# Kernel tuning notes

Measured on AMD Instinct MI355X. Metric: run time of the kernel, lower is better.

## Reference

```python
import jax, jax.numpy as jnp
import numpy as np

B, T, C = 2, 2048, 1024
H, GAMMA = 16, 8
D = C // H
SCALE = 1.0 / np.sqrt(D).astype(np.float32)


def setup_inputs() -> dict:
    key = jax.random.key(0)
    ks = jax.random.split(key, 6)
    w = 0.02
    return {
        'x': jax.random.normal(ks[0], (B, T, C), dtype=jnp.float32),
        'Wq': jax.random.normal(ks[1], (C, 2 * C), dtype=jnp.float32) * w,
        'Wk': jax.random.normal(ks[2], (C, 2 * C), dtype=jnp.float32) * w,
        'Wv': jax.random.normal(ks[3], (C, C), dtype=jnp.float32) * w,
        'Wo': jax.random.normal(ks[4], (C, C), dtype=jnp.float32) * w,
        'theta_offset': jax.random.normal(ks[5], (H,), dtype=jnp.float32) * 0.1,
    }


def _heads(t):
    # (B, T, C) -> (B, H, T, D)
    return t.reshape(B, T, H, D).transpose(0, 2, 1, 3)


def reference(x, Wq, Wk, Wv, Wo, theta_offset):
    q_raw = x @ Wq                      # (B, T, 2C)
    k_raw = x @ Wk                      # (B, T, 2C)
    v = _heads(x @ Wv)                  # (B, H, T, D)

    q_amp, q_phase = jnp.split(q_raw, 2, axis=-1)
    k_amp, k_phase = jnp.split(k_raw, 2, axis=-1)
    q_amp = jax.nn.softplus(_heads(q_amp))
    q_phase = _heads(q_phase)
    k_amp = jax.nn.softplus(_heads(k_amp))
    k_phase = _heads(k_phase)

    q_real = q_amp * jnp.cos(q_phase)
    q_imag = q_amp * jnp.sin(q_phase)
    k_real = k_amp * jnp.cos(k_phase)
    k_imag = k_amp * jnp.sin(k_phase)

    scores = (jnp.einsum('bhtd,bhsd->bhts', q_real, k_real)
              + jnp.einsum('bhtd,bhsd->bhts', q_imag, k_imag)) * SCALE

    # theta gating (active since T > GAMMA)
    cycle_ids = jnp.arange(T, dtype=jnp.float32) / GAMMA
    cycle_dist = cycle_ids[None, :] - cycle_ids[:, None]        # (T, T)
    theta_gate = jnp.cos(theta_offset[:, None, None] * cycle_dist)  # (H, T, T)
    scores = scores * theta_gate[None]

    causal = jnp.tril(jnp.ones((T, T), dtype=bool))
    scores = jnp.where(causal[None, None], scores, -jnp.inf)
    attn = jax.nn.softmax(scores, axis=-1)

    out = jnp.einsum('bhts,bhsd->bhtd', attn, v)
    out = out.transpose(0, 2, 1, 3).reshape(B, T, C)
    return out @ Wo
```

## Files before the change

kernel.cpp:

```cpp
#include <hip/hip_runtime.h>
#include <hip/hip_bf16.h>
#include <math.h>

#define Bc 2
#define Tc 2048
#define Cc 1024
#define Hc 16
#define Dc 64

typedef __attribute__((ext_vector_type(8))) short short8;
typedef __attribute__((ext_vector_type(4))) float f32x4;

#define L2E 1.44269504088896f
#define SM_M 20.0f

__device__ __forceinline__ short f2bf(float x) {
    unsigned u = __float_as_uint(x);
    u += 0x7fff + ((u >> 16) & 1);
    return (short)(u >> 16);
}
__device__ __forceinline__ unsigned pack2bf_fast(float a, float b) {
    unsigned ua = __float_as_uint(a) + 0x8000u;
    unsigned ub = __float_as_uint(b) + 0x8000u;
    return __builtin_amdgcn_perm(ub, ua, 0x07060302);
}
__device__ __forceinline__ float softplus_fast(float a) {
    return fmaxf(a, 0.f) + __logf(1.f + __expf(-fabsf(a)));
}

#define RDA(BUF, MH) do {                                                      \
    const short* Ah_ = &Al[BUF][MH][0];                                        \
    _Pragma("unroll") for (int mt_ = 0; mt_ < 4; ++mt_) {                      \
        af[mt_][0] = *(const short8*)&Ah_[(wm*64 + mt_*16 + c)*64 + rsw0];     \
        af[mt_][1] = *(const short8*)&Ah_[(wm*64 + mt_*16 + c)*64 + rsw1];     \
    } } while (0)

#define RDB(BUF, NH) do {                                                      \
    const short* Bh_ = &Bl[BUF][NH][0];                                        \
    _Pragma("unroll") for (int nf_ = 0; nf_ < 2; ++nf_) {                      \
        bfr[NH][nf_][0] = *(const short8*)&Bh_[(wn*32 + nf_*16 + c)*64 + rsw0];\
        bfr[NH][nf_][1] = *(const short8*)&Bh_[(wn*32 + nf_*16 + c)*64 + rsw1];\
    } } while (0)

#define MMQ(MH, NH) do {                                                       \
    _Pragma("unroll") for (int mt_ = 0; mt_ < 4; ++mt_)                        \
    _Pragma("unroll") for (int nf_ = 0; nf_ < 2; ++nf_) {                      \
        acc[MH][NH][mt_][nf_] = __builtin_amdgcn_mfma_f32_16x16x32_bf16(       \
            af[mt_][0], bfr[NH][nf_][0], acc[MH][NH][mt_][nf_], 0, 0, 0);      \
        acc[MH][NH][mt_][nf_] = __builtin_amdgcn_mfma_f32_16x16x32_bf16(       \
            af[mt_][1], bfr[NH][nf_][1], acc[MH][NH][mt_][nf_], 0, 0, 0);      \
    } } while (0)

#define BARw asm volatile("s_barrier" ::: "memory")
#define VMW6 asm volatile("s_waitcnt vmcnt(6)" ::: "memory")
#define VMW0 asm volatile("s_waitcnt vmcnt(0)" ::: "memory")
#define PRIO1 __builtin_amdgcn_s_setprio(1)
#define PRIO0 __builtin_amdgcn_s_setprio(0)

__global__ __launch_bounds__(512, 2) void gemm256_qk(
    const short* __restrict__ A, const short* __restrict__ Bt,
    short* __restrict__ q2, short* __restrict__ k2)
{
    __shared__ __attribute__((aligned(16))) short Al[2][2][128 * 64];
    __shared__ __attribute__((aligned(16))) short Bl[2][2][128 * 64];

    const int tid = threadIdx.x;
    const int wave = tid >> 6, lane = tid & 63;
    const int quad = lane >> 4, c = lane & 15;
    const int wm = wave >> 2, wn = wave & 3;
    const int m0 = blockIdx.y * 256, n0 = blockIdx.x * 256;

    const int rsw0 = ((quad * 16) ^ ((c & 7) << 4)) >> 1;
    const int rsw1 = ((64 + quad * 16) ^ ((c & 7) << 4)) >> 1;

    f32x4 acc[2][2][4][2];
#pragma unroll
    for (int a0 = 0; a0 < 2; ++a0)
#pragma unroll
        for (int a1 = 0; a1 < 2; ++a1)
#pragma unroll
            for (int a2 = 0; a2 < 4; ++a2)
#pragma unroll
                for (int a3 = 0; a3 < 2; ++a3)
                    acc[a0][a1][a2][a3] = (f32x4){0.f, 0.f, 0.f, 0.f};

    short8 af[4][2];
    short8 bfr[2][2][2];

    auto stA = [&](int kt, int hh) {
        short* dstb = &Al[kt & 1][hh][0];
#pragma unroll
        for (int j = 0; j < 2; ++j) {
            int ch = j * 512 + tid;
            int row = ch >> 3;
            int os = ((((ch & 7) << 4) ^ ((row & 7) << 4)) >> 1);
            const short* src = A + (size_t)(m0 + hh * 128 + row) * 1024 + kt * 64 + os;
            __builtin_amdgcn_global_load_lds(
                (const __attribute__((address_space(1))) void*)src,
                (__attribute__((address_space(3))) void*)(dstb + (j * 512 + wave * 64) * 8),
                16, 0, 0);
        }
    };
    auto stB = [&](int kt, int hh) {
        short* dstb = &Bl[kt & 1][hh][0];
#pragma unroll
        for (int j = 0; j < 2; ++j) {
            int ch = j * 512 + tid;
            int row = ch >> 3;
            int os = ((((ch & 7) << 4) ^ ((row & 7) << 4)) >> 1);
            const short* src = Bt + (size_t)(n0 + hh * 128 + row) * 1024 + kt * 64 + os;
            __builtin_amdgcn_global_load_lds(
                (const __attribute__((address_space(1))) void*)src,
                (__attribute__((address_space(3))) void*)(dstb + (j * 512 + wave * 64) * 8),
                16, 0, 0);
        }
    };

    stB(0, 0); stA(0, 0); stB(0, 1); stA(0, 1); stB(1, 0); stA(1, 0); stB(1, 1);
    VMW6;
    BARw;

    for (int i = 0; i < 8; ++i) {
        const int e = 2 * i;
        const bool more = (i < 7);
        RDA(0, 0); RDB(0, 0);
        stA(e + 1, 1);
        BARw; PRIO1; MMQ(0, 0); PRIO0; BARw;
        RDB(0, 1);
        if (more) stB(e + 2, 0);
        BARw; PRIO1; MMQ(0, 1); PRIO0; BARw;
        RDA(0, 1);
        if (more) stA(e + 2, 0);
        BARw; PRIO1; MMQ(1, 0); PRIO0; BARw;
        if (more) stB(e + 2, 1);
        BARw; PRIO1; MMQ(1, 1); PRIO0;
        if (more) { VMW6; } else { VMW0; }
        BARw;
        RDA(1, 0); RDB(1, 0);
        if (more) stA(e + 2, 1);
        BARw; PRIO1; MMQ(0, 0); PRIO0; BARw;
        RDB(1, 1);
        if (more) stB(e + 3, 0);
        BARw; PRIO1; MMQ(0, 1); PRIO0; BARw;
        RDA(1, 1);
        if (more) stA(e + 3, 0);
        BARw; PRIO1; MMQ(1, 0); PRIO0; BARw;
        if (more) stB(e + 3, 1);
        BARw; PRIO1; MMQ(1, 1); PRIO0;
        if (more) { VMW6; } else { VMW0; }
        BARw;
    }

    const int bx = blockIdx.x;
    const int d = wn * 16 + c;
#pragma unroll
    for (int mh = 0; mh < 2; ++mh) {
#pragma unroll
        for (int nh = 0; nh < 2; ++nh) {
            const int g = 2 * bx + nh;
            const int isK = g >> 4;
            const int hh = g & 15;
            const float scl = isK ? 1.f : 0.125f;
            short* dst = isK ? k2 : q2;
#pragma unroll
            for (int mt = 0; mt < 4; ++mt) {
#pragma unroll
                for (int reg = 0; reg < 4; ++reg) {
                    int m = m0 + mh * 128 + wm * 64 + mt * 16 + quad * 4 + reg;
                    int bb = m >> 11, tt = m & (Tc - 1);
                    size_t base = (((size_t)bb * Hc + hh) * Tc + tt) * 128;
                    float amp = acc[mh][nh][mt][0][reg];
                    float ph  = acc[mh][nh][mt][1][reg];
                    float sp = softplus_fast(amp) * scl;
                    float sn, cs;
                    __sincosf(ph, &sn, &cs);
                    dst[base + d]      = f2bf(sp * cs);
                    dst[base + d + 64] = f2bf(sp * sn);
                }
            }
        }
    }
}

template <int EPI>
__global__ __launch_bounds__(256) void gemm_bt_mfma(
    const short* __restrict__ A, const short* __restrict__ Bt,
    float* __restrict__ Cf, short* __restrict__ Cb,
    int M, int N, int K)
{
    __shared__ __attribute__((aligned(16))) short As[128 * 32];
    __shared__ __attribute__((aligned(16))) short Bs[128 * 32];

    const int tid = threadIdx.x;
    const int wave = tid >> 6, lane = tid & 63;
    const int quad = lane >> 4, c = lane & 15;
    const int wm = wave >> 1, wn = wave & 1;
    const int m0 = blockIdx.y * 128, n0 = blockIdx.x * 128;

    const int srow = lane >> 2;
    const int scol = (lane & 3) * 8;
    const short* Ag = A  + (size_t)(m0 + wave * 32 + srow) * K + scol;
    const short* Bg = Bt + (size_t)(n0 + wave * 32 + srow) * K + scol;
    short* AsW = As + (wave * 32) * 32;
    short* BsW = Bs + (wave * 32) * 32;

    f32x4 acc[4][4];
#pragma unroll
    for (int i = 0; i < 4; ++i)
#pragma unroll
        for (int j = 0; j < 4; ++j)
            acc[i][j] = (f32x4){0.f, 0.f, 0.f, 0.f};

    for (int k0 = 0; k0 < K; k0 += 32) {
        __syncthreads();
#pragma unroll
        for (int i = 0; i < 2; ++i) {
            __builtin_amdgcn_global_load_lds(
                (const __attribute__((address_space(1))) void*)(Ag + k0 + (size_t)i * 16 * K),
                (__attribute__((address_space(3))) void*)(AsW + i * 16 * 32), 16, 0, 0);
            __builtin_amdgcn_global_load_lds(
                (const __attribute__((address_space(1))) void*)(Bg + k0 + (size_t)i * 16 * K),
                (__attribute__((address_space(3))) void*)(BsW + i * 16 * 32), 16, 0, 0);
        }
        __syncthreads();

        short8 af[4], bf[4];
#pragma unroll
        for (int mt = 0; mt < 4; ++mt)
            af[mt] = *(const short8*)&As[(wm * 64 + mt * 16 + c) * 32 + quad * 8];
#pragma unroll
        for (int nt = 0; nt < 4; ++nt)
            bf[nt] = *(const short8*)&Bs[(wn * 64 + nt * 16 + c) * 32 + quad * 8];
#pragma unroll
        for (int mt = 0; mt < 4; ++mt)
#pragma unroll
            for (int nt = 0; nt < 4; ++nt)
                acc[mt][nt] = __builtin_amdgcn_mfma_f32_16x16x32_bf16(
                    af[mt], bf[nt], acc[mt][nt], 0, 0, 0);
    }

#pragma unroll
    for (int mt = 0; mt < 4; ++mt) {
#pragma unroll
        for (int reg = 0; reg < 4; ++reg) {
            size_t row = m0 + wm * 64 + mt * 16 + quad * 4 + reg;
#pragma unroll
            for (int nt = 0; nt < 4; ++nt) {
                size_t col = n0 + wn * 64 + nt * 16 + c;
                if (EPI == 1) Cb[row * N + col] = f2bf(acc[mt][nt][reg]);
                else          Cf[row * N + col] = acc[mt][nt][reg];
            }
        }
    }
}

__global__ __launch_bounds__(256) void gemm_v2t(
    const short* __restrict__ A, const short* __restrict__ Bt,
    short* __restrict__ v2t)
{
    __shared__ __attribute__((aligned(16))) short As[128 * 32];
    __shared__ __attribute__((aligned(16))) short Bs[128 * 32];
    __shared__ __attribute__((aligned(16))) short tile[128 * 136];

    const int K = Cc;
    const int tid = threadIdx.x;
    const int wave = tid >> 6, lane = tid & 63;
    const int quad = lane >> 4, c = lane & 15;
    const int wm = wave >> 1, wn = wave & 1;
    const int m0 = blockIdx.y * 128, n0 = blockIdx.x * 128;

    const int srow = lane >> 2;
    const int scol = (lane & 3) * 8;
    const short* Ag = A  + (size_t)(m0 + wave * 32 + srow) * K + scol;
    const short* Bg = Bt + (size_t)(n0 + wave * 32 + srow) * K + scol;
    short* AsW = As + (wave * 32) * 32;
    short* BsW = Bs + (wave * 32) * 32;

    f32x4 acc[4][4];
#pragma unroll
    for (int i = 0; i < 4; ++i)
#pragma unroll
        for (int j = 0; j < 4; ++j)
            acc[i][j] = (f32x4){0.f, 0.f, 0.f, 0.f};

    for (int k0 = 0; k0 < K; k0 += 32) {
        __syncthreads();
#pragma unroll
        for (int i = 0; i < 2; ++i) {
            __builtin_amdgcn_global_load_lds(
                (const __attribute__((address_space(1))) void*)(Ag + k0 + (size_t)i * 16 * K),
                (__attribute__((address_space(3))) void*)(AsW + i * 16 * 32), 16, 0, 0);
            __builtin_amdgcn_global_load_lds(
                (const __attribute__((address_space(1))) void*)(Bg + k0 + (size_t)i * 16 * K),
                (__attribute__((address_space(3))) void*)(BsW + i * 16 * 32), 16, 0, 0);
        }
        __syncthreads();

        short8 af[4], bf[4];
#pragma unroll
        for (int mt = 0; mt < 4; ++mt)
            af[mt] = *(const short8*)&As[(wm * 64 + mt * 16 + c) * 32 + quad * 8];
#pragma unroll
        for (int nt = 0; nt < 4; ++nt)
            bf[nt] = *(const short8*)&Bs[(wn * 64 + nt * 16 + c) * 32 + quad * 8];
#pragma unroll
        for (int mt = 0; mt < 4; ++mt)
#pragma unroll
            for (int nt = 0; nt < 4; ++nt)
                acc[mt][nt] = __builtin_amdgcn_mfma_f32_16x16x32_bf16(
                    af[mt], bf[nt], acc[mt][nt], 0, 0, 0);
    }

#pragma unroll
    for (int mt = 0; mt < 4; ++mt)
#pragma unroll
        for (int reg = 0; reg < 4; ++reg) {
            int tl = wm * 64 + mt * 16 + quad * 4 + reg;
#pragma unroll
            for (int nt = 0; nt < 4; ++nt)
                tile[(wn * 64 + nt * 16 + c) * 136 + tl] = f2bf(acc[mt][nt][reg]);
        }
    __syncthreads();

    const int b = m0 >> 11, tl0 = m0 & (Tc - 1);
#pragma unroll
    for (int i = 0; i < 8; ++i) {
        int n = i * 16 + (tid >> 4);
        int t8 = (tid & 15) * 8;
        int ng = n0 + n, h = ng >> 6, d = ng & 63;
        *(short8*)&v2t[(((size_t)b * Hc + h) * Dc + d) * Tc + tl0 + t8] =
            *(const short8*)&tile[n * 136 + t8];
    }
}

__global__ __launch_bounds__(256) void xconv(const float* __restrict__ x,
                                             short* __restrict__ xb)
{
    int idx = blockIdx.x * 256 + threadIdx.x;
    float4 v = *(const float4*)&x[(size_t)idx * 4];
    short4 o = {f2bf(v.x), f2bf(v.y), f2bf(v.z), f2bf(v.w)};
    *(short4*)&xb[(size_t)idx * 4] = o;
}

__global__ __launch_bounds__(256) void wtrans_qk(const float* __restrict__ Wq,
                                                 const float* __restrict__ Wk,
                                                 short* __restrict__ Bt)
{
    __shared__ short tile[64][80];
    const int n0 = blockIdx.x * 64, k0 = blockIdx.y * 64;
    const int half = blockIdx.z;
    const float* W = half ? Wk : Wq;
    const int tid = threadIdx.x;
#pragma unroll
    for (int i = 0; i < 4; ++i) {
        int e = i * 256 + tid;
        int k = e >> 4, n4 = (e & 15) * 4;
        float4 v = *(const float4*)&W[(size_t)(k0 + k) * 2048 + n0 + n4];
        tile[k][n4]     = f2bf(v.x);
        tile[k][n4 + 1] = f2bf(v.y);
        tile[k][n4 + 2] = f2bf(v.z);
        tile[k][n4 + 3] = f2bf(v.w);
    }
    __syncthreads();
#pragma unroll
    for (int i = 0; i < 16; ++i) {
        int e = i * 256 + tid;
        int n = e >> 6, k = e & 63;
        int ng = n0 + n;
        int sub = ng >> 10, hh = (ng >> 6) & 15, dd = ng & 63;
        int r = (half * 16 + hh) * 128 + (dd >> 4) * 32 + sub * 16 + (dd & 15);
        Bt[(size_t)r * Cc + k0 + k] = tile[k][n];
    }
}

__global__ __launch_bounds__(256) void wtrans2(const float* __restrict__ Wv,
                                               const float* __restrict__ Wo,
                                               short* __restrict__ WtBase)
{
    __shared__ short tile[64][80];
    const int n0 = blockIdx.x * 64, k0 = blockIdx.y * 64;
    const float* W = blockIdx.z ? Wo : Wv;
    short* Wt = WtBase + (size_t)blockIdx.z * Cc * Cc;
    const int tid = threadIdx.x;
#pragma unroll
    for (int i = 0; i < 4; ++i) {
        int e = i * 256 + tid;
        int k = e >> 4, n4 = (e & 15) * 4;
        float4 v = *(const float4*)&W[(size_t)(k0 + k) * Cc + n0 + n4];
        tile[k][n4]     = f2bf(v.x);
        tile[k][n4 + 1] = f2bf(v.y);
        tile[k][n4 + 2] = f2bf(v.z);
        tile[k][n4 + 3] = f2bf(v.w);
    }
    __syncthreads();
#pragma unroll
    for (int i = 0; i < 16; ++i) {
        int e = i * 256 + tid;
        int n = e >> 6, k = e & 63;
        Wt[(size_t)(n0 + n) * Cc + k0 + k] = tile[k][n];
    }
}

__global__ __launch_bounds__(512, 4) void moire_attn6(
    const short* __restrict__ q2, const short* __restrict__ k2,
    const short* __restrict__ v2t, const float* __restrict__ theta,
    short* __restrict__ att)
{
    __shared__ __attribute__((aligned(16))) short Ks[2][64 * 128];
    __shared__ __attribute__((aligned(16))) short Vt[2][64 * 64];
    __shared__ __attribute__((aligned(16))) short Ps[8][16 * 64];

    const int tid = threadIdx.x;
    const int wave = tid >> 6, lane = tid & 63;
    const int quad = lane >> 4, c = lane & 15;
    const int tx = wave >> 2, wq = wave & 3;
    const int p = blockIdx.x, h = blockIdx.y, b = blockIdx.z;
    const int qx = tx ? (31 - p) : p;
    const int q0 = qx * 64;
    const float th = theta[h];

    const short* k2b = k2 + (size_t)(b * Hc + h) * Tc * 128;
    const short* v2b = v2t + (size_t)(b * Hc + h) * Dc * Tc;

    short8 qf[4];
    const short* qp = q2 + ((size_t)(b * Hc + h) * Tc + q0 + wq * 16 + c) * 128;
#pragma unroll
    for (int i = 0; i < 4; ++i)
        qf[i] = *(const short8*)(qp + i * 32 + quad * 8);

    const int t_l = wq * 16 + c;
    float x0 = th * 0.125f * (float)(q0 + t_l);
    float cb = __cosf(x0), sb = -__sinf(x0);
    float cOff[4][4], sOff[4][4];
#pragma unroll
    for (int mt = 0; mt < 4; ++mt)
#pragma unroll
        for (int reg = 0; reg < 4; ++reg) {
            float a = th * 0.125f * (float)(mt * 16 + quad * 4 + reg);
            cOff[mt][reg] = __cosf(a) * L2E;
            sOff[mt][reg] = __sinf(a) * L2E;
        }
    const float cD = __cosf(8.f * th), sD = __sinf(8.f * th);

    f32x4 oacc[4];
    float lsum = 0.f;
#pragma unroll
    for (int nt = 0; nt < 4; ++nt)
        oacc[nt] = (f32x4){0.f, 0.f, 0.f, 0.f};

    auto stageK = [&](int jts) {
        short* KsB = &Ks[jts & 1][0];
        const int s0 = jts * 64;
#pragma unroll
        for (int i = 0; i < 2; ++i) {
            int ch = i * 512 + tid;
            int row = ch >> 4, j = ch & 15;
            const short* src = k2b + (size_t)(s0 + row) * 128 + ((j ^ (row & 15)) << 3);
            __builtin_amdgcn_global_load_lds(
                (const __attribute__((address_space(1))) void*)src,
                (__attribute__((address_space(3))) void*)(KsB + (i * 512 + wave * 64) * 8),
                16, 0, 0);
        }
    };
    auto stageV = [&](int jts) {
        short* VtB = &Vt[jts & 1][0];
        const int s0 = jts * 64;
        int row = tid >> 3, j = tid & 7;
        const short* src = v2b + (size_t)row * Tc + s0 + ((j ^ (row & 7)) << 3);
        __builtin_amdgcn_global_load_lds(
            (const __attribute__((address_space(1))) void*)src,
            (__attribute__((address_space(3))) void*)(VtB + (wave * 64) * 8),
            16, 0, 0);
    };

    auto do_pv = [&](int jprev) {
        const short* VtB = &Vt[jprev & 1][0];
        short8 pf[2];
#pragma unroll
        for (int kk = 0; kk < 2; ++kk)
            pf[kk] = *(const short8*)&Ps[wave][c * 64 +
                         (((kk * 4 + quad) ^ (c & 7)) << 3)];
#pragma unroll
        for (int nt = 0; nt < 4; ++nt)
#pragma unroll
            for (int kk = 0; kk < 2; ++kk) {
                short8 vf = *(const short8*)&VtB[(nt * 16 + c) * 64 +
                             (((kk * 4 + quad) ^ (c & 7)) << 3)];
                oacc[nt] = __builtin_amdgcn_mfma_f32_16x16x32_bf16(
                    pf[kk], vf, oacc[nt], 0, 0, 0);
            }
    };

    auto do_s = [&](int jt) {
        const short* KsB = &Ks[jt & 1][0];
        const bool diag = (jt == qx);

        f32x4 s_acc[4];
#pragma unroll
        for (int mt = 0; mt < 4; ++mt) {
            f32x4 a = {0.f, 0.f, 0.f, 0.f};
#pragma unroll
            for (int kk = 0; kk < 4; ++kk) {
                short8 kf = *(const short8*)&KsB[(mt * 16 + c) * 128 +
                                                 (((kk * 4 + quad) ^ c) << 3)];
                a = __builtin_amdgcn_mfma_f32_16x16x32_bf16(kf, qf[kk], a, 0, 0, 0);
            }
            s_acc[mt] = a;
        }

#pragma unroll
        for (int mt = 0; mt < 4; ++mt) {
            float pv[4];
#pragma unroll
            for (int reg = 0; reg < 4; ++reg) {
                float g2 = cb * cOff[mt][reg] - sb * sOff[mt][reg];
                float arg = fmaf(s_acc[mt][reg], g2, -SM_M * L2E);
                if (diag && (mt * 16 + quad * 4 + reg) > t_l) arg = -1e30f;
                pv[reg] = exp2f(arg);
            }
            lsum += (pv[0] + pv[1]) + (pv[2] + pv[3]);
            uint2 pk = {pack2bf_fast(pv[0], pv[1]), pack2bf_fast(pv[2], pv[3])};
            int slot = ((mt * 2 + (quad >> 1)) ^ (c & 7));
            *(uint2*)&Ps[wave][c * 64 + slot * 8 + (quad & 1) * 4] = pk;
        }

        float ncb = cb * cD - sb * sD;
        sb = sb * cD + cb * sD;
        cb = ncb;
    };

    stageK(0);
    const int jtEnd = 31 - p;
    for (int jt = 0; jt <= jtEnd; ++jt) {
        __syncthreads();
        if (jt < jtEnd) stageK(jt + 1);
        stageV(jt);

        const bool doS  = (jt <= qx);
        const bool doPV = (jt >= 1) & (jt <= qx + 1);
        if (doS & doPV) {
            do_pv(jt - 1);
            do_s(jt);
        } else if (doS) {
            do_s(jt);
        } else if (doPV) {
            do_pv(jt - 1);
        }
    }

    __syncthreads();
    if (qx == jtEnd) do_pv(jtEnd);

    float l = lsum;
    l += __shfl_xor(l, 16);
    l += __shfl_xor(l, 32);
    float il = 1.f / l;
    float ilr[4];
#pragma unroll
    for (int reg = 0; reg < 4; ++reg)
        ilr[reg] = __shfl(il, quad * 4 + reg);
#pragma unroll
    for (int reg = 0; reg < 4; ++reg) {
        int t_g = q0 + wq * 16 + quad * 4 + reg;
#pragma unroll
        for (int nt = 0; nt < 4; ++nt)
            att[(size_t)(b * Tc + t_g) * Cc + h * Dc + nt * 16 + c] =
                f2bf(oacc[nt][reg] * ilr[reg]);
    }
}

extern "C" void kernel_launch(void* const* d_in, const int* in_sizes, int n_in,
                              void* d_out, int out_size, void* d_ws, size_t ws_size,
                              hipStream_t stream)
{
    const float* x     = (const float*)d_in[0];
    const float* Wq    = (const float*)d_in[1];
    const float* Wk    = (const float*)d_in[2];
    const float* Wv    = (const float*)d_in[3];
    const float* Wo    = (const float*)d_in[4];
    const float* theta = (const float*)d_in[5];
    float* out = (float*)d_out;

    const int M = Bc * Tc;
    char* ws = (char*)d_ws;
    const size_t MB = 1 << 20;
    short* xb   = (short*)(ws);
    short* Bqk  = (short*)(ws + 8 * MB);
    short* Wvt  = (short*)(ws + 16 * MB);
    short* Wot  = (short*)(ws + 18 * MB);
    short* v2t  = (short*)(ws + 28 * MB);
    short* attb = (short*)(ws + 36 * MB);
    short* q2   = (short*)(ws + 44 * MB);
    short* k2   = (short*)d_out;

    xconv<<<(size_t)M * Cc / 1024, 256, 0, stream>>>(x, xb);
    wtrans_qk<<<dim3(2048 / 64, Cc / 64, 2), 256, 0, stream>>>(Wq, Wk, Bqk);
    wtrans2<<<dim3(Cc / 64, Cc / 64, 2), 256, 0, stream>>>(Wv, Wo, Wvt);

    gemm256_qk<<<dim3(4096 / 256, M / 256), 512, 0, stream>>>(xb, Bqk, q2, k2);
    gemm_v2t<<<dim3(Cc / 128, M / 128), 256, 0, stream>>>(xb, Wvt, v2t);

    moire_attn6<<<dim3(16, Hc, Bc), 512, 0, stream>>>(q2, k2, v2t, theta, attb);

    gemm_bt_mfma<0><<<dim3(Cc / 128, M / 128), 256, 0, stream>>>(
        attb, Wot, out, nullptr, M, Cc, Cc);
}
```

Baseline: 245.9 us.

## Split attention KV range across two wave groups per query tile

```diff
diff --git a/kernel.cpp b/kernel.cpp
--- a/kernel.cpp
+++ b/kernel.cpp
@@ -401,21 +401,21 @@
     }
 }
 
-__global__ __launch_bounds__(512, 4) void moire_attn6(
+__global__ __launch_bounds__(512, 4) void moire_attn7(
     const short* __restrict__ q2, const short* __restrict__ k2,
     const short* __restrict__ v2t, const float* __restrict__ theta,
     short* __restrict__ att)
 {
-    __shared__ __attribute__((aligned(16))) short Ks[2][64 * 128];
-    __shared__ __attribute__((aligned(16))) short Vt[2][64 * 64];
-    __shared__ __attribute__((aligned(16))) short Ps[8][16 * 64];
+    __shared__ __attribute__((aligned(16))) short Ks[2][2][32 * 128];
+    __shared__ __attribute__((aligned(16))) short Vt[2][2][64 * 32];
+    __shared__ __attribute__((aligned(16))) short Ps[8][16 * 32];
 
     const int tid = threadIdx.x;
     const int wave = tid >> 6, lane = tid & 63;
     const int quad = lane >> 4, c = lane & 15;
-    const int tx = wave >> 2, wq = wave & 3;
-    const int p = blockIdx.x, h = blockIdx.y, b = blockIdx.z;
-    const int qx = tx ? (31 - p) : p;
+    const int tx = wave >> 2, gw = wave & 3;
+    const int qx = 31 - blockIdx.x;
+    const int h = blockIdx.y, b = blockIdx.z;
     const int q0 = qx * 64;
     const float th = theta[h];
 
@@ -423,24 +423,26 @@
     const short* v2b = v2t + (size_t)(b * Hc + h) * Dc * Tc;
 
     short8 qf[4];
-    const short* qp = q2 + ((size_t)(b * Hc + h) * Tc + q0 + wq * 16 + c) * 128;
+    const short* qp = q2 + ((size_t)(b * Hc + h) * Tc + q0 + gw * 16 + c) * 128;
 #pragma unroll
     for (int i = 0; i < 4; ++i)
         qf[i] = *(const short8*)(qp + i * 32 + quad * 8);
 
-    const int t_l = wq * 16 + c;
-    float x0 = th * 0.125f * (float)(q0 + t_l);
-    float cb = __cosf(x0), sb = -__sinf(x0);
-    float cOff[4][4], sOff[4][4];
-#pragma unroll
-    for (int mt = 0; mt < 4; ++mt)
+    const int t_l = gw * 16 + c;
+    const int t_g = q0 + t_l;
+    const int sBase = tx * (qx + 1);
+    float x0 = th * 0.125f * (32.f * (float)sBase - (float)t_g);
+    float cb = __cosf(x0), sb = __sinf(x0);
+    float cOff[2][4], sOff[2][4];
+#pragma unroll
+    for (int mt = 0; mt < 2; ++mt)
 #pragma unroll
         for (int reg = 0; reg < 4; ++reg) {
             float a = th * 0.125f * (float)(mt * 16 + quad * 4 + reg);
             cOff[mt][reg] = __cosf(a) * L2E;
             sOff[mt][reg] = __sinf(a) * L2E;
         }
-    const float cD = __cosf(8.f * th), sD = __sinf(8.f * th);
+    const float cD = __cosf(4.f * th), sD = __sinf(4.f * th);
 
     f32x4 oacc[4];
     float lsum = 0.f;
@@ -448,56 +450,38 @@
     for (int nt = 0; nt < 4; ++nt)
         oacc[nt] = (f32x4){0.f, 0.f, 0.f, 0.f};
 
-    auto stageK = [&](int jts) {
-        short* KsB = &Ks[jts & 1][0];
-        const int s0 = jts * 64;
-#pragma unroll
-        for (int i = 0; i < 2; ++i) {
-            int ch = i * 512 + tid;
+    auto stageK = [&](int s_i, int buf) {
+        short* dst = &Ks[tx][buf][0];
+#pragma unroll
+        for (int jj = 0; jj < 2; ++jj) {
+            int ch = jj * 256 + gw * 64 + lane;
             int row = ch >> 4, j = ch & 15;
-            const short* src = k2b + (size_t)(s0 + row) * 128 + ((j ^ (row & 15)) << 3);
+            const short* src = k2b + (size_t)(s_i * 32 + row) * 128 +
+                               ((j ^ (row & 15)) << 3);
             __builtin_amdgcn_global_load_lds(
                 (const __attribute__((address_space(1))) void*)src,
-                (__attribute__((address_space(3))) void*)(KsB + (i * 512 + wave * 64) * 8),
+                (__attribute__((address_space(3))) void*)(dst + (jj * 256 + gw * 64) * 8),
                 16, 0, 0);
         }
     };
-    auto stageV = [&](int jts) {
-        short* VtB = &Vt[jts & 1][0];
-        const int s0 = jts * 64;
-        int row = tid >> 3, j = tid & 7;
-        const short* src = v2b + (size_t)row * Tc + s0 + ((j ^ (row & 7)) << 3);
+    auto stageV = [&](int s_i, int buf) {
+        short* dst = &Vt[tx][buf][0];
+        int ch = gw * 64 + lane;
+        int d = ch >> 2, j = ch & 3;
+        const short* src = v2b + (size_t)d * Tc + s_i * 32 + ((j ^ (d & 3)) << 3);
         __builtin_amdgcn_global_load_lds(
             (const __attribute__((address_space(1))) void*)src,
-            (__attribute__((address_space(3))) void*)(VtB + (wave * 64) * 8),
+            (__attribute__((address_space(3))) void*)(dst + (gw * 64) * 8),
             16, 0, 0);
     };
 
-    auto do_pv = [&](int jprev) {
-        const short* VtB = &Vt[jprev & 1][0];
-        short8 pf[2];
-#pragma unroll
-        for (int kk = 0; kk < 2; ++kk)
-            pf[kk] = *(const short8*)&Ps[wave][c * 64 +
-                         (((kk * 4 + quad) ^ (c & 7)) << 3)];
-#pragma unroll
-        for (int nt = 0; nt < 4; ++nt)
-#pragma unroll
-            for (int kk = 0; kk < 2; ++kk) {
-                short8 vf = *(const short8*)&VtB[(nt * 16 + c) * 64 +
-                             (((kk * 4 + quad) ^ (c & 7)) << 3)];
-                oacc[nt] = __builtin_amdgcn_mfma_f32_16x16x32_bf16(
-                    pf[kk], vf, oacc[nt], 0, 0, 0);
-            }
-    };
-
-    auto do_s = [&](int jt) {
-        const short* KsB = &Ks[jt & 1][0];
-        const bool diag = (jt == qx);
-
-        f32x4 s_acc[4];
-#pragma unroll
-        for (int mt = 0; mt < 4; ++mt) {
+    auto do_s = [&](int s_i, int buf) {
+        const short* KsB = &Ks[tx][buf][0];
+        const bool maycross = (s_i >= 2 * qx);
+
+        f32x4 s_acc[2];
+#pragma unroll
+        for (int mt = 0; mt < 2; ++mt) {
             f32x4 a = {0.f, 0.f, 0.f, 0.f};
 #pragma unroll
             for (int kk = 0; kk < 4; ++kk) {
@@ -509,19 +493,20 @@
         }
 
 #pragma unroll
-        for (int mt = 0; mt < 4; ++mt) {
+        for (int mt = 0; mt < 2; ++mt) {
             float pv[4];
 #pragma unroll
             for (int reg = 0; reg < 4; ++reg) {
                 float g2 = cb * cOff[mt][reg] - sb * sOff[mt][reg];
                 float arg = fmaf(s_acc[mt][reg], g2, -SM_M * L2E);
-                if (diag && (mt * 16 + quad * 4 + reg) > t_l) arg = -1e30f;
+                if (maycross && (s_i * 32 + mt * 16 + quad * 4 + reg) > t_g)
+                    arg = -1e30f;
                 pv[reg] = exp2f(arg);
             }
             lsum += (pv[0] + pv[1]) + (pv[2] + pv[3]);
             uint2 pk = {pack2bf_fast(pv[0], pv[1]), pack2bf_fast(pv[2], pv[3])};
-            int slot = ((mt * 2 + (quad >> 1)) ^ (c & 7));
-            *(uint2*)&Ps[wave][c * 64 + slot * 8 + (quad & 1) * 4] = pk;
+            int slot = (mt * 2 + (quad >> 1)) ^ (c & 3);
+            *(uint2*)&Ps[wave][c * 32 + slot * 8 + (quad & 1) * 4] = pk;
         }
 
         float ncb = cb * cD - sb * sD;
@@ -529,43 +514,64 @@
         cb = ncb;
     };
 
-    stageK(0);
-    const int jtEnd = 31 - p;
-    for (int jt = 0; jt <= jtEnd; ++jt) {
+    auto do_pv = [&](int buf) {
+        const short* VtB = &Vt[tx][buf][0];
+        short8 pf = *(const short8*)&Ps[wave][c * 32 + ((quad ^ (c & 3)) << 3)];
+#pragma unroll
+        for (int nt = 0; nt < 4; ++nt) {
+            short8 vf = *(const short8*)&VtB[(nt * 16 + c) * 32 +
+                                             ((quad ^ (c & 3)) << 3)];
+            oacc[nt] = __builtin_amdgcn_mfma_f32_16x16x32_bf16(
+                pf, vf, oacc[nt], 0, 0, 0);
+        }
+    };
+
+    const int nIt = qx + 1;
+    stageK(sBase, 0); stageV(sBase, 0);
+    for (int i = 0; i < nIt; ++i) {
         __syncthreads();
-        if (jt < jtEnd) stageK(jt + 1);
-        stageV(jt);
-
-        const bool doS  = (jt <= qx);
-        const bool doPV = (jt >= 1) & (jt <= qx + 1);
-        if (doS & doPV) {
-            do_pv(jt - 1);
-            do_s(jt);
-        } else if (doS) {
-            do_s(jt);
-        } else if (doPV) {
-            do_pv(jt - 1);
-        }
+        if (i + 1 < nIt) {
+            stageK(sBase + i + 1, (i + 1) & 1);
+            stageV(sBase + i + 1, (i + 1) & 1);
+        }
+        do_s(sBase + i, i & 1);
+        do_pv(i & 1);
     }
 
     __syncthreads();
-    if (qx == jtEnd) do_pv(jtEnd);
-
-    float l = lsum;
-    l += __shfl_xor(l, 16);
-    l += __shfl_xor(l, 32);
-    float il = 1.f / l;
-    float ilr[4];
-#pragma unroll
-    for (int reg = 0; reg < 4; ++reg)
-        ilr[reg] = __shfl(il, quad * 4 + reg);
-#pragma unroll
-    for (int reg = 0; reg < 4; ++reg) {
-        int t_g = q0 + wq * 16 + quad * 4 + reg;
-#pragma unroll
-        for (int nt = 0; nt < 4; ++nt)
-            att[(size_t)(b * Tc + t_g) * Cc + h * Dc + nt * 16 + c] =
-                f2bf(oacc[nt][reg] * ilr[reg]);
+    float* Cmb = (float*)&Ks[0][0][0];
+    if (tx == 1) {
+        float* pp = Cmb + (size_t)(gw * 64 + lane) * 20;
+#pragma unroll
+        for (int nt = 0; nt < 4; ++nt) *(f32x4*)(pp + nt * 4) = oacc[nt];
+        pp[16] = lsum;
+    }
+    __syncthreads();
+    if (tx == 0) {
+        const float* pp = Cmb + (size_t)(gw * 64 + lane) * 20;
+#pragma unroll
+        for (int nt = 0; nt < 4; ++nt) {
+            f32x4 t = *(const f32x4*)(pp + nt * 4);
+            oacc[nt] += t;
+        }
+        lsum += pp[16];
+
+        float l = lsum;
+        l += __shfl_xor(l, 16);
+        l += __shfl_xor(l, 32);
+        float il = 1.f / l;
+        float ilr[4];
+#pragma unroll
+        for (int reg = 0; reg < 4; ++reg)
+            ilr[reg] = __shfl(il, quad * 4 + reg);
+#pragma unroll
+        for (int reg = 0; reg < 4; ++reg) {
+            int t_o = q0 + gw * 16 + quad * 4 + reg;
+#pragma unroll
+            for (int nt = 0; nt < 4; ++nt)
+                att[(size_t)(b * Tc + t_o) * Cc + h * Dc + nt * 16 + c] =
+                    f2bf(oacc[nt][reg] * ilr[reg]);
+        }
     }
 }
 
@@ -600,7 +606,7 @@
     gemm256_qk<<<dim3(4096 / 256, M / 256), 512, 0, stream>>>(xb, Bqk, q2, k2);
     gemm_v2t<<<dim3(Cc / 128, M / 128), 256, 0, stream>>>(xb, Wvt, v2t);
 
-    moire_attn6<<<dim3(16, Hc, Bc), 512, 0, stream>>>(q2, k2, v2t, theta, attb);
+    moire_attn7<<<dim3(32, Hc, Bc), 512, 0, stream>>>(q2, k2, v2t, theta, attb);
 
     gemm_bt_mfma<0><<<dim3(Cc / 128, M / 128), 256, 0, stream>>>(
         attb, Wot, out, nullptr, M, Cc, Cc);
```

Result: slower. 294.0 us (+19.6%).

## Rebalance attention block work by splitting long query tile across both wave groups

Applied to the files above, without the earlier changes.

```diff
diff --git a/kernel.cpp b/kernel.cpp
--- a/kernel.cpp
+++ b/kernel.cpp
@@ -401,7 +401,7 @@
     }
 }
 
-__global__ __launch_bounds__(512, 4) void moire_attn6(
+__global__ __launch_bounds__(512, 4) void moire_attn8(
     const short* __restrict__ q2, const short* __restrict__ k2,
     const short* __restrict__ v2t, const float* __restrict__ theta,
     short* __restrict__ att)
@@ -413,22 +413,27 @@
     const int tid = threadIdx.x;
     const int wave = tid >> 6, lane = tid & 63;
     const int quad = lane >> 4, c = lane & 15;
-    const int tx = wave >> 2, wq = wave & 3;
+    const int tx = wave >> 2, gw = wave & 3;
     const int p = blockIdx.x, h = blockIdx.y, b = blockIdx.z;
-    const int qx = tx ? (31 - p) : p;
-    const int q0 = qx * 64;
+    const int qB = 31 - p;
     const float th = theta[h];
 
     const short* k2b = k2 + (size_t)(b * Hc + h) * Tc * 128;
     const short* v2b = v2t + (size_t)(b * Hc + h) * Dc * Tc;
+    const short* q2b = q2 + (size_t)(b * Hc + h) * Tc * 128;
+
+    int qcur = tx ? qB : p;
+    int q0 = qcur * 64;
+    const int t_l = gw * 16 + c;
 
     short8 qf[4];
-    const short* qp = q2 + ((size_t)(b * Hc + h) * Tc + q0 + wq * 16 + c) * 128;
-#pragma unroll
-    for (int i = 0; i < 4; ++i)
-        qf[i] = *(const short8*)(qp + i * 32 + quad * 8);
-
-    const int t_l = wq * 16 + c;
+    {
+        const short* qp = q2b + (size_t)(q0 + t_l) * 128;
+#pragma unroll
+        for (int i = 0; i < 4; ++i)
+            qf[i] = *(const short8*)(qp + i * 32 + quad * 8);
+    }
+
     float x0 = th * 0.125f * (float)(q0 + t_l);
     float cb = __cosf(x0), sb = -__sinf(x0);
     float cOff[4][4], sOff[4][4];
@@ -448,8 +453,8 @@
     for (int nt = 0; nt < 4; ++nt)
         oacc[nt] = (f32x4){0.f, 0.f, 0.f, 0.f};
 
-    auto stageK = [&](int jts) {
-        short* KsB = &Ks[jts & 1][0];
+    auto stageK_all = [&](int jts, int buf) {
+        short* dst = &Ks[buf][0];
         const int s0 = jts * 64;
 #pragma unroll
         for (int i = 0; i < 2; ++i) {
@@ -458,42 +463,50 @@
             const short* src = k2b + (size_t)(s0 + row) * 128 + ((j ^ (row & 15)) << 3);
             __builtin_amdgcn_global_load_lds(
                 (const __attribute__((address_space(1))) void*)src,
-                (__attribute__((address_space(3))) void*)(KsB + (i * 512 + wave * 64) * 8),
+                (__attribute__((address_space(3))) void*)(dst + (i * 512 + wave * 64) * 8),
                 16, 0, 0);
         }
     };
-    auto stageV = [&](int jts) {
-        short* VtB = &Vt[jts & 1][0];
+    auto stageV_all = [&](int jts, int buf) {
+        short* dst = &Vt[buf][0];
         const int s0 = jts * 64;
         int row = tid >> 3, j = tid & 7;
         const short* src = v2b + (size_t)row * Tc + s0 + ((j ^ (row & 7)) << 3);
         __builtin_amdgcn_global_load_lds(
             (const __attribute__((address_space(1))) void*)src,
-            (__attribute__((address_space(3))) void*)(VtB + (wave * 64) * 8),
+            (__attribute__((address_space(3))) void*)(dst + (wave * 64) * 8),
             16, 0, 0);
     };
-
-    auto do_pv = [&](int jprev) {
-        const short* VtB = &Vt[jprev & 1][0];
-        short8 pf[2];
-#pragma unroll
-        for (int kk = 0; kk < 2; ++kk)
-            pf[kk] = *(const short8*)&Ps[wave][c * 64 +
-                         (((kk * 4 + quad) ^ (c & 7)) << 3)];
-#pragma unroll
-        for (int nt = 0; nt < 4; ++nt)
-#pragma unroll
-            for (int kk = 0; kk < 2; ++kk) {
-                short8 vf = *(const short8*)&VtB[(nt * 16 + c) * 64 +
-                             (((kk * 4 + quad) ^ (c & 7)) << 3)];
-                oacc[nt] = __builtin_amdgcn_mfma_f32_16x16x32_bf16(
-                    pf[kk], vf, oacc[nt], 0, 0, 0);
-            }
-    };
-
-    auto do_s = [&](int jt) {
-        const short* KsB = &Ks[jt & 1][0];
-        const bool diag = (jt == qx);
+    auto stage_grp = [&](int jts, int buf) {
+        const int s0 = jts * 64;
+        const int ltid = tid & 255;
+        short* dk = &Ks[buf][0];
+#pragma unroll
+        for (int jj = 0; jj < 4; ++jj) {
+            int ch = jj * 256 + ltid;
+            int row = ch >> 4, j = ch & 15;
+            const short* src = k2b + (size_t)(s0 + row) * 128 + ((j ^ (row & 15)) << 3);
+            __builtin_amdgcn_global_load_lds(
+                (const __attribute__((address_space(1))) void*)src,
+                (__attribute__((address_space(3))) void*)(dk + (jj * 256 + gw * 64) * 8),
+                16, 0, 0);
+        }
+        short* dv = &Vt[buf][0];
+#pragma unroll
+        for (int jj = 0; jj < 2; ++jj) {
+            int ch = jj * 256 + ltid;
+            int row = ch >> 3, j = ch & 7;
+            const short* src = v2b + (size_t)row * Tc + s0 + ((j ^ (row & 7)) << 3);
+            __builtin_amdgcn_global_load_lds(
+                (const __attribute__((address_space(1))) void*)src,
+                (__attribute__((address_space(3))) void*)(dv + (jj * 256 + gw * 64) * 8),
+                16, 0, 0);
+        }
+    };
+
+    auto do_s = [&](int jt, int buf) {
+        const short* KsB = &Ks[buf][0];
+        const bool diag = (jt == qcur);
 
         f32x4 s_acc[4];
 #pragma unroll
@@ -529,43 +542,98 @@
         cb = ncb;
     };
 
-    stageK(0);
-    const int jtEnd = 31 - p;
-    for (int jt = 0; jt <= jtEnd; ++jt) {
+    auto do_pv = [&](int buf) {
+        const short* VtB = &Vt[buf][0];
+        short8 pf[2];
+#pragma unroll
+        for (int kk = 0; kk < 2; ++kk)
+            pf[kk] = *(const short8*)&Ps[wave][c * 64 +
+                         (((kk * 4 + quad) ^ (c & 7)) << 3)];
+#pragma unroll
+        for (int nt = 0; nt < 4; ++nt)
+#pragma unroll
+            for (int kk = 0; kk < 2; ++kk) {
+                short8 vf = *(const short8*)&VtB[(nt * 16 + c) * 64 +
+                             (((kk * 4 + quad) ^ (c & 7)) << 3)];
+                oacc[nt] = __builtin_amdgcn_mfma_f32_16x16x32_bf16(
+                    pf[kk], vf, oacc[nt], 0, 0, 0);
+            }
+    };
+
+    auto write_out = [&]() {
+        float l = lsum;
+        l += __shfl_xor(l, 16);
+        l += __shfl_xor(l, 32);
+        float il = 1.f / l;
+        float ilr[4];
+#pragma unroll
+        for (int reg = 0; reg < 4; ++reg)
+            ilr[reg] = __shfl(il, quad * 4 + reg);
+#pragma unroll
+        for (int reg = 0; reg < 4; ++reg) {
+            int t_o = q0 + gw * 16 + quad * 4 + reg;
+#pragma unroll
+            for (int nt = 0; nt < 4; ++nt)
+                att[(size_t)(b * Tc + t_o) * Cc + h * Dc + nt * 16 + c] =
+                    f2bf(oacc[nt][reg] * ilr[reg]);
+        }
+    };
+
+    stageK_all(0, 0); stageV_all(0, 0);
+    for (int jt = 0; jt <= p; ++jt) {
         __syncthreads();
-        if (jt < jtEnd) stageK(jt + 1);
-        stageV(jt);
-
-        const bool doS  = (jt <= qx);
-        const bool doPV = (jt >= 1) & (jt <= qx + 1);
-        if (doS & doPV) {
-            do_pv(jt - 1);
-            do_s(jt);
-        } else if (doS) {
-            do_s(jt);
-        } else if (doPV) {
-            do_pv(jt - 1);
-        }
-    }
+        stageK_all(jt + 1, (jt + 1) & 1);
+        stageV_all(jt + 1, (jt + 1) & 1);
+        do_s(jt, jt & 1);
+        do_pv(jt & 1);
+    }
+    const int slotB = (p + 1) & 1, slotA = slotB ^ 1;
 
     __syncthreads();
-    if (qx == jtEnd) do_pv(jtEnd);
-
-    float l = lsum;
-    l += __shfl_xor(l, 16);
-    l += __shfl_xor(l, 32);
-    float il = 1.f / l;
-    float ilr[4];
-#pragma unroll
-    for (int reg = 0; reg < 4; ++reg)
-        ilr[reg] = __shfl(il, quad * 4 + reg);
-#pragma unroll
-    for (int reg = 0; reg < 4; ++reg) {
-        int t_g = q0 + wq * 16 + quad * 4 + reg;
+    if (tx == 0) {
+        write_out();
 #pragma unroll
         for (int nt = 0; nt < 4; ++nt)
-            att[(size_t)(b * Tc + t_g) * Cc + h * Dc + nt * 16 + c] =
-                f2bf(oacc[nt][reg] * ilr[reg]);
+            oacc[nt] = (f32x4){0.f, 0.f, 0.f, 0.f};
+        lsum = 0.f;
+        qcur = qB; q0 = qB * 64;
+        const short* qp = q2b + (size_t)(q0 + t_l) * 128;
+#pragma unroll
+        for (int i = 0; i < 4; ++i)
+            qf[i] = *(const short8*)(qp + i * 32 + quad * 8);
+        float a = th * 0.125f * (1088.f - (float)(q0 + t_l));
+        __sincosf(a, &sb, &cb);
+    } else {
+        do_s(p + 1, slotB);
+        do_pv(slotB);
+    }
+
+    for (int i = 0; i <= 14 - p; ++i) {
+        const int jt = tx ? (p + 2 + i) : (17 + i);
+        const int sl = tx ? slotB : slotA;
+        __syncthreads();
+        stage_grp(jt, sl);
+        __syncthreads();
+        do_s(jt, sl);
+        do_pv(sl);
+    }
+
+    __syncthreads();
+    float* Cmb = (float*)&Ks[0][0];
+    if (tx == 0) {
+        float* pp = Cmb + (size_t)(gw * 64 + lane) * 20;
+#pragma unroll
+        for (int nt = 0; nt < 4; ++nt) *(f32x4*)(pp + nt * 4) = oacc[nt];
+        pp[16] = lsum;
+    }
+    __syncthreads();
+    if (tx == 1) {
+        const float* pp = Cmb + (size_t)(gw * 64 + lane) * 20;
+#pragma unroll
+        for (int nt = 0; nt < 4; ++nt)
+            oacc[nt] += *(const f32x4*)(pp + nt * 4);
+        lsum += pp[16];
+        write_out();
     }
 }
 
@@ -600,7 +668,7 @@
     gemm256_qk<<<dim3(4096 / 256, M / 256), 512, 0, stream>>>(xb, Bqk, q2, k2);
     gemm_v2t<<<dim3(Cc / 128, M / 128), 256, 0, stream>>>(xb, Wvt, v2t);
 
-    moire_attn6<<<dim3(16, Hc, Bc), 512, 0, stream>>>(q2, k2, v2t, theta, attb);
+    moire_attn8<<<dim3(16, Hc, Bc), 512, 0, stream>>>(q2, k2, v2t, theta, attb);
 
     gemm_bt_mfma<0><<<dim3(Cc / 128, M / 128), 256, 0, stream>>>(
         attb, Wot, out, nullptr, M, Cc, Cc);
```

New measurement: 236.3 us. 1.04x faster.
